# Performance work log

Hardware: AMD Instinct MI355X
Metric: run time of the kernel (lower is better)

## Reference

```python
import jax, jax.numpy as jnp
import numpy as np

HIDDEN = 1024
HEADS = 16
HEAD_DIM = HIDDEN // HEADS
SCALE = HEAD_DIM ** -0.5


def setup_inputs() -> dict:
    key = jax.random.key(0)
    kx, kw, ko = jax.random.split(key, 3)
    x = jax.random.normal(kx, (2, 2048, HIDDEN), dtype=jnp.float32)
    # nn.Linear(hidden, 3*hidden, bias=False): weight shape [3*hidden, hidden]
    w_qkv = jax.random.normal(kw, (3 * HIDDEN, HIDDEN), dtype=jnp.float32) * (HIDDEN ** -0.5)
    w_out = jax.random.normal(ko, (HIDDEN, HIDDEN), dtype=jnp.float32) * (HIDDEN ** -0.5)
    return {"x": x, "w_qkv": w_qkv, "w_out": w_out}


def reference(x, w_qkv, w_out):
    b, s, d = x.shape
    qkv = jnp.einsum('bsd,ed->bse', x, w_qkv)  # [b,s,3d]
    q, k, v = jnp.split(qkv, 3, axis=-1)
    def heads(t):
        return t.reshape(b, s, HEADS, HEAD_DIM).transpose(0, 2, 1, 3)  # [b,h,s,hd]
    q, k, v = heads(q), heads(k), heads(v)
    scores = jnp.einsum('bhqd,bhkd->bhqk', q, k) * SCALE
    attn = jax.nn.softmax(scores, axis=-1)
    out = jnp.einsum('bhqk,bhkd->bhqd', attn, v)
    out = out.transpose(0, 2, 1, 3).reshape(b, s, d)
    return jnp.einsum('bsd,ed->bse', out, w_out)
```

## Files before the change

### kernel.cpp

```cpp
#include <hip/hip_runtime.h>
#include <hip/hip_bf16.h>
#include <stdint.h>

typedef __bf16 bf16;
typedef __bf16 bf16x8 __attribute__((ext_vector_type(8)));
typedef float f32x4 __attribute__((ext_vector_type(4)));

#define HIDDEN 1024
#define HEADS  16
#define HD     64
#define SEQ    2048
#define BATCH  2
#define NTOK   (BATCH*SEQ)
#define E3     (3*HIDDEN)

#define QSCALE (0.125f * 1.44269504088896f)

#if __has_builtin(__builtin_amdgcn_exp2f)
#define EXP2(x) __builtin_amdgcn_exp2f(x)
#else
#define EXP2(x) __expf((x) * 0.69314718055995f)
#endif

static __device__ __forceinline__ uint32_t pkbf(float a, float b) {
  union { bf16 h[2]; uint32_t u; } x;
  x.h[0] = (bf16)a; x.h[1] = (bf16)b;
  return x.u;
}

__global__ __launch_bounds__(256) void k_convert(
    const float* __restrict__ x, const float* __restrict__ wqkv, const float* __restrict__ wout,
    bf16* __restrict__ xb, bf16* __restrict__ wqkvb, bf16* __restrict__ woutb)
{
  const int NX = NTOK*HIDDEN/4, NW = E3*HIDDEN/4;
  int i = blockIdx.x*256 + threadIdx.x;
  const float4* s; bf16* d; int o;
  if (i < NX)            { s=(const float4*)x;    d=xb;    o=i; }
  else if (i < NX+NW)    { s=(const float4*)wqkv; d=wqkvb; o=i-NX; }
  else                   { s=(const float4*)wout; d=woutb; o=i-NX-NW; }
  float4 v = s[o];
  union { bf16 b[4]; uint2 u; } p;
  p.b[0]=(bf16)v.x; p.b[1]=(bf16)v.y; p.b[2]=(bf16)v.z; p.b[3]=(bf16)v.w;
  *(uint2*)(d + (size_t)o*4) = p.u;
}

template<int EPI, int BM>
__global__ __launch_bounds__(256) void k_gemm(
    const bf16* __restrict__ A, const bf16* __restrict__ B,
    bf16* __restrict__ Oq, bf16* __restrict__ Ok, bf16* __restrict__ Ov,
    float* __restrict__ Of, int M, int N, int K, int nbn)
{
  constexpr int MI = BM/32;
  __shared__ bf16 As[BM*32];
  __shared__ bf16 Bs[128*32];
  const int t = threadIdx.x;
  const int lane = t & 63;
  const int w = t >> 6;
  const int g = lane >> 4;
  const int l15 = lane & 15;
  const int wm = (w >> 1) * (BM/2), wn = (w & 1) * 64;
  const int bm = blockIdx.x / nbn, bn = blockIdx.x % nbn;
  const int brow = bm*BM, bcol = bn*128;

  f32x4 acc[MI][4];
  #pragma unroll
  for (int mi=0;mi<MI;mi++)
    #pragma unroll
    for (int ni=0;ni<4;ni++)
      #pragma unroll
      for (int r=0;r<4;r++) acc[mi][ni][r] = 0.f;

  const int nk = K >> 5;
  for (int kt = 0; kt < nk; ++kt) {
    if constexpr (BM == 128) {
      int ch = w*128 + lane;
      const bf16* ga = A + (size_t)(brow + (ch>>2))*K + kt*32 + (ch&3)*8;
      __builtin_amdgcn_global_load_lds((const uint32_t*)ga, (uint32_t*)(As + (w*128)*8), 16, 0, 0);
      int ch2 = ch + 64;
      const bf16* ga2 = A + (size_t)(brow + (ch2>>2))*K + kt*32 + (ch2&3)*8;
      __builtin_amdgcn_global_load_lds((const uint32_t*)ga2, (uint32_t*)(As + (w*128+64)*8), 16, 0, 0);
    } else {
      int ch = w*64 + lane;
      const bf16* ga = A + (size_t)(brow + (ch>>2))*K + kt*32 + (ch&3)*8;
      __builtin_amdgcn_global_load_lds((const uint32_t*)ga, (uint32_t*)(As + (w*64)*8), 16, 0, 0);
    }
    {
      int ch = w*128 + lane;
      const bf16* gb = B + (size_t)(bcol + (ch>>2))*K + kt*32 + (ch&3)*8;
      __builtin_amdgcn_global_load_lds((const uint32_t*)gb, (uint32_t*)(Bs + (w*128)*8), 16, 0, 0);
      int ch2 = ch + 64;
      const bf16* gb2 = B + (size_t)(bcol + (ch2>>2))*K + kt*32 + (ch2&3)*8;
      __builtin_amdgcn_global_load_lds((const uint32_t*)gb2, (uint32_t*)(Bs + (w*128+64)*8), 16, 0, 0);
    }
    __syncthreads();
    bf16x8 af[MI], bfr[4];
    #pragma unroll
    for (int mi=0;mi<MI;mi++) af[mi]  = *(const bf16x8*)(As + (wm + mi*16 + l15)*32 + g*8);
    #pragma unroll
    for (int ni=0;ni<4;ni++) bfr[ni] = *(const bf16x8*)(Bs + (wn + ni*16 + l15)*32 + g*8);
    #pragma unroll
    for (int mi=0;mi<MI;mi++)
      #pragma unroll
      for (int ni=0;ni<4;ni++)
        acc[mi][ni] = __builtin_amdgcn_mfma_f32_16x16x32_bf16(af[mi], bfr[ni], acc[mi][ni], 0, 0, 0);
    __syncthreads();
  }

  #pragma unroll
  for (int mi=0;mi<MI;mi++) {
    #pragma unroll
    for (int ni=0;ni<4;ni++) {
      #pragma unroll
      for (int r=0;r<4;r++) {
        float val = acc[mi][ni][r];
        int m = brow + wm + mi*16 + 4*g + r;
        int e = bcol + wn + ni*16 + l15;
        if (EPI == 0) {
          int part = e >> 10, we = e & 1023;
          int hh = we >> 6, dd = we & 63;
          int b = m >> 11, sb = m & 2047;
          size_t idx = (((size_t)b*HEADS + hh)*SEQ + sb)*HD + dd;
          if (part == 0)      Oq[idx] = (bf16)(val * QSCALE);
          else if (part == 1) Ok[idx] = (bf16)val;
          else                Ov[idx] = (bf16)val;
        } else {
          Of[(size_t)m*HIDDEN + e] = val;
        }
      }
    }
  }
}

__global__ __launch_bounds__(256, 4) void k_attn(
    const bf16* __restrict__ Qg, const bf16* __restrict__ Kg, const bf16* __restrict__ Vg,
    bf16* __restrict__ Og)
{
  __shared__ bf16 Kl[64*64];
  __shared__ bf16 Vt[64*64];
  const int t = threadIdx.x;
  const int lane = t & 63;
  const int w = t >> 6;
  const int g = lane >> 4;
  const int q = lane & 15;
  const int bh = blockIdx.x >> 5;
  const int qb = blockIdx.x & 31;
  const int q0 = qb*64 + w*16;
  const size_t bhS = (size_t)bh * SEQ * HD;

  bf16x8 qf[2];
  {
    const bf16* qrow = Qg + bhS + (size_t)(q0 + q)*HD + 8*g;
    qf[0] = *(const bf16x8*)(qrow);
    qf[1] = *(const bf16x8*)(qrow + 32);
  }

  f32x4 ot[4];
  #pragma unroll
  for (int df=0;df<4;df++)
    #pragma unroll
    for (int r=0;r<4;r++) ot[df][r] = 0.f;
  float mrun = -3.0e38f, lrun = 0.f;

  const int kv0 = (t & 31)*2;
  const int dd0 = (t >> 5)*8;
  const int kvf0 = kv0 >> 4, gv = (kv0 >> 2) & 3, rv = kv0 & 3;
  const int pos0 = 32*(kvf0 >> 1) + 8*gv + 4*(kvf0 & 1) + rv;

  for (int it = 0; it < SEQ/64; ++it) {
    __syncthreads();
    {
      int ch = w*128 + lane;
      int row = ch>>3, o16 = ch&7;
      const bf16* gp = Kg + bhS + (size_t)(it*64+row)*HD + ((o16*8) ^ ((row&7)*8));
      __builtin_amdgcn_global_load_lds((const uint32_t*)gp, (uint32_t*)(Kl + (w*128)*8), 16, 0, 0);
      int ch2 = ch + 64;
      int row2 = ch2>>3, o16b = ch2&7;
      const bf16* gp2 = Kg + bhS + (size_t)(it*64+row2)*HD + ((o16b*8) ^ ((row2&7)*8));
      __builtin_amdgcn_global_load_lds((const uint32_t*)gp2, (uint32_t*)(Kl + (w*128+64)*8), 16, 0, 0);
    }
    {
      const bf16* vg = Vg + bhS + (size_t)(it*64 + kv0)*HD + dd0;
      uint4 va = *(const uint4*)vg;
      uint4 vb = *(const uint4*)(vg + HD);
      const uint32_t* pa = (const uint32_t*)&va;
      const uint32_t* pb = (const uint32_t*)&vb;
      #pragma unroll
      for (int jj=0;jj<8;jj++) {
        int dd = dd0 + jj;
        uint32_t pr = __builtin_amdgcn_perm(pb[jj>>1], pa[jj>>1],
                                            (jj&1) ? 0x07060302u : 0x05040100u);
        int byte = (dd*128 + pos0*2) ^ (jj<<4);
        *(uint32_t*)((char*)Vt + byte) = pr;
      }
    }
    __syncthreads();

    f32x4 sf[4];
    #pragma unroll
    for (int kvf=0;kvf<4;kvf++)
      #pragma unroll
      for (int r=0;r<4;r++) sf[kvf][r] = 0.f;
    #pragma unroll
    for (int kvf=0;kvf<4;kvf++) {
      int row = 16*kvf + q;
      #pragma unroll
      for (int kc=0;kc<2;kc++) {
        int byte = row*128 + (((16*g + 64*kc)) ^ ((row&7)<<4));
        bf16x8 kf = *(const bf16x8*)((const char*)Kl + byte);
        sf[kvf] = __builtin_amdgcn_mfma_f32_16x16x32_bf16(kf, qf[kc], sf[kvf], 0,0,0);
      }
    }

    float pm = -3.0e38f;
    #pragma unroll
    for (int kvf=0;kvf<4;kvf++)
      #pragma unroll
      for (int r=0;r<4;r++) pm = fmaxf(pm, sf[kvf][r]);
    pm = fmaxf(pm, __shfl_xor(pm, 16, 64));
    pm = fmaxf(pm, __shfl_xor(pm, 32, 64));

    if (__any(pm - mrun > 8.f)) {
      float mnew = fmaxf(mrun, pm);
      float alpha = EXP2(mrun - mnew);
      lrun *= alpha;
      #pragma unroll
      for (int df=0;df<4;df++)
        #pragma unroll
        for (int r=0;r<4;r++) ot[df][r] *= alpha;
      mrun = mnew;
    }
    float rs = 0.f;
    #pragma unroll
    for (int kvf=0;kvf<4;kvf++)
      #pragma unroll
      for (int r=0;r<4;r++) { float p = EXP2(sf[kvf][r]-mrun); sf[kvf][r]=p; rs += p; }
    rs += __shfl_xor(rs, 16, 64);
    rs += __shfl_xor(rs, 32, 64);
    lrun += rs;

    uint32_t pk[4][2];
    #pragma unroll
    for (int kvf=0;kvf<4;kvf++) {
      pk[kvf][0] = pkbf(sf[kvf][0], sf[kvf][1]);
      pk[kvf][1] = pkbf(sf[kvf][2], sf[kvf][3]);
    }

    #pragma unroll
    for (int kc=0;kc<2;kc++) {
      union { uint32_t u[4]; bf16x8 v; } pf;
      pf.u[0] = pk[2*kc][0]; pf.u[1] = pk[2*kc][1];
      pf.u[2] = pk[2*kc+1][0]; pf.u[3] = pk[2*kc+1][1];
      #pragma unroll
      for (int df=0;df<4;df++) {
        int row = 16*df + q;
        int byte = row*128 + (((16*g + 64*kc)) ^ ((row&7)<<4));
        bf16x8 vf = *(const bf16x8*)((const char*)Vt + byte);
        ot[df] = __builtin_amdgcn_mfma_f32_16x16x32_bf16(vf, pf.v, ot[df], 0,0,0);
      }
    }
  }

  float inv = 1.0f / lrun;
  int b = bh >> 4, head = bh & 15;
  size_t orow = ((size_t)b*SEQ + q0 + q)*HIDDEN + head*HD;
  #pragma unroll
  for (int df=0;df<4;df++) {
    uint2 pr;
    pr.x = pkbf(ot[df][0]*inv, ot[df][1]*inv);
    pr.y = pkbf(ot[df][2]*inv, ot[df][3]*inv);
    *(uint2*)(Og + orow + 16*df + 4*g) = pr;
  }
}

extern "C" void kernel_launch(void* const* d_in, const int* in_sizes, int n_in,
                              void* d_out, int out_size, void* d_ws, size_t ws_size,
                              hipStream_t stream)
{
  (void)in_sizes; (void)n_in; (void)out_size; (void)ws_size;
  const float* x    = (const float*)d_in[0];
  const float* wqkv = (const float*)d_in[1];
  const float* wout = (const float*)d_in[2];
  float* out = (float*)d_out;
  char* ws = (char*)d_ws;
  bf16* xb    = (bf16*)(ws);
  bf16* wqkvb = (bf16*)(ws + 8388608);
  bf16* woutb = (bf16*)(ws + 14680064);
  bf16* Q     = (bf16*)(ws + 16777216);
  bf16* K     = (bf16*)(ws + 25165824);
  bf16* V     = (bf16*)(ws + 33554432);
  bf16* O     = (bf16*)(ws + 41943040);

  k_convert<<<8192, 256, 0, stream>>>(x, wqkv, wout, xb, wqkvb, woutb);
  k_gemm<0,128><<<32*24, 256, 0, stream>>>(xb, wqkvb, Q, K, V, nullptr, NTOK, E3, HIDDEN, 24);
  k_attn<<<1024, 256, 0, stream>>>(Q, K, V, O);
  k_gemm<1,64><<<64*8, 256, 0, stream>>>(O, woutb, nullptr, nullptr, nullptr, out, NTOK, HIDDEN, HIDDEN, 8);
}
```

Before: 204.3 us.

## Double query rows per wave in attention and prefetch next K/V tile into registers

Each wave now handles 32 query rows instead of 16, so every K and V fragment read from LDS feeds two MFMAs and the block count is halved. The K load changes from direct global-to-LDS copies to register loads that are issued for the next tile right after the barrier, overlapping global latency with compute. In exchange the kernel uses more registers, with launch bounds lowered to 2 blocks per SM, and has fewer blocks in flight.

```diff
diff --git a/kernel.cpp b/kernel.cpp
--- a/kernel.cpp
+++ b/kernel.cpp
@@ -131,7 +131,7 @@
   }
 }
 
-__global__ __launch_bounds__(256, 4) void k_attn(
+__global__ __launch_bounds__(256, 2) void k_attn(
     const bf16* __restrict__ Qg, const bf16* __restrict__ Kg, const bf16* __restrict__ Vg,
     bf16* __restrict__ Og)
 {
@@ -142,133 +142,172 @@
   const int w = t >> 6;
   const int g = lane >> 4;
   const int q = lane & 15;
-  const int bh = blockIdx.x >> 5;
-  const int qb = blockIdx.x & 31;
-  const int q0 = qb*64 + w*16;
+  const int bh = blockIdx.x >> 4;
+  const int qb = blockIdx.x & 15;
+  const int q0 = qb*128 + w*32;
   const size_t bhS = (size_t)bh * SEQ * HD;
 
-  bf16x8 qf[2];
-  {
-    const bf16* qrow = Qg + bhS + (size_t)(q0 + q)*HD + 8*g;
-    qf[0] = *(const bf16x8*)(qrow);
-    qf[1] = *(const bf16x8*)(qrow + 32);
-  }
-
-  f32x4 ot[4];
-  #pragma unroll
-  for (int df=0;df<4;df++)
-    #pragma unroll
-    for (int r=0;r<4;r++) ot[df][r] = 0.f;
-  float mrun = -3.0e38f, lrun = 0.f;
-
+  bf16x8 qf[2][2];
+  #pragma unroll
+  for (int qs=0;qs<2;qs++) {
+    const bf16* qrow = Qg + bhS + (size_t)(q0 + 16*qs + q)*HD + 8*g;
+    qf[qs][0] = *(const bf16x8*)(qrow);
+    qf[qs][1] = *(const bf16x8*)(qrow + 32);
+  }
+
+  f32x4 ot[2][4];
+  #pragma unroll
+  for (int qs=0;qs<2;qs++)
+    #pragma unroll
+    for (int df=0;df<4;df++)
+      #pragma unroll
+      for (int r=0;r<4;r++) ot[qs][df][r] = 0.f;
+  float mrun0 = -3.0e38f, mrun1 = -3.0e38f, lrun0 = 0.f, lrun1 = 0.f;
+
+  const int kr0 = t >> 3, kp0 = t & 7;
   const int kv0 = (t & 31)*2;
   const int dd0 = (t >> 5)*8;
   const int kvf0 = kv0 >> 4, gv = (kv0 >> 2) & 3, rv = kv0 & 3;
   const int pos0 = 32*(kvf0 >> 1) + 8*gv + 4*(kvf0 & 1) + rv;
 
-  for (int it = 0; it < SEQ/64; ++it) {
+  auto loadK = [&](int it, uint4& a, uint4& b) {
+    const bf16* p0 = Kg + bhS + (size_t)(it*64 + kr0)*HD + kp0*8;
+    a = *(const uint4*)p0;
+    b = *(const uint4*)(p0 + 32*HD);
+  };
+  auto writeK = [&](uint4 a, uint4 b) {
+    int sw = (kp0 ^ (kr0 & 7)) * 16;
+    *(uint4*)((char*)Kl + kr0*128 + sw) = a;
+    *(uint4*)((char*)Kl + (kr0+32)*128 + sw) = b;
+  };
+  auto loadV = [&](int it, uint4& a, uint4& b) {
+    const bf16* vg = Vg + bhS + (size_t)(it*64 + kv0)*HD + dd0;
+    a = *(const uint4*)vg;
+    b = *(const uint4*)(vg + HD);
+  };
+  auto writeVt = [&](uint4 va, uint4 vb) {
+    const uint32_t* pa = (const uint32_t*)&va;
+    const uint32_t* pb = (const uint32_t*)&vb;
+    #pragma unroll
+    for (int jj=0;jj<8;jj++) {
+      int dd = dd0 + jj;
+      uint32_t pr = __builtin_amdgcn_perm(pb[jj>>1], pa[jj>>1],
+                                          (jj&1) ? 0x07060302u : 0x05040100u);
+      int byte = (dd*128 + pos0*2) ^ (jj<<4);
+      *(uint32_t*)((char*)Vt + byte) = pr;
+    }
+  };
+
+  uint4 ka, kb, va, vb;
+  loadK(0, ka, kb);
+  loadV(0, va, vb);
+
+  const int NT = SEQ/64;
+  for (int it = 0; it < NT; ++it) {
     __syncthreads();
-    {
-      int ch = w*128 + lane;
-      int row = ch>>3, o16 = ch&7;
-      const bf16* gp = Kg + bhS + (size_t)(it*64+row)*HD + ((o16*8) ^ ((row&7)*8));
-      __builtin_amdgcn_global_load_lds((const uint32_t*)gp, (uint32_t*)(Kl + (w*128)*8), 16, 0, 0);
-      int ch2 = ch + 64;
-      int row2 = ch2>>3, o16b = ch2&7;
-      const bf16* gp2 = Kg + bhS + (size_t)(it*64+row2)*HD + ((o16b*8) ^ ((row2&7)*8));
-      __builtin_amdgcn_global_load_lds((const uint32_t*)gp2, (uint32_t*)(Kl + (w*128+64)*8), 16, 0, 0);
-    }
-    {
-      const bf16* vg = Vg + bhS + (size_t)(it*64 + kv0)*HD + dd0;
-      uint4 va = *(const uint4*)vg;
-      uint4 vb = *(const uint4*)(vg + HD);
-      const uint32_t* pa = (const uint32_t*)&va;
-      const uint32_t* pb = (const uint32_t*)&vb;
-      #pragma unroll
-      for (int jj=0;jj<8;jj++) {
-        int dd = dd0 + jj;
-        uint32_t pr = __builtin_amdgcn_perm(pb[jj>>1], pa[jj>>1],
-                                            (jj&1) ? 0x07060302u : 0x05040100u);
-        int byte = (dd*128 + pos0*2) ^ (jj<<4);
-        *(uint32_t*)((char*)Vt + byte) = pr;
-      }
-    }
+    writeK(ka, kb);
+    writeVt(va, vb);
     __syncthreads();
-
-    f32x4 sf[4];
-    #pragma unroll
-    for (int kvf=0;kvf<4;kvf++)
-      #pragma unroll
-      for (int r=0;r<4;r++) sf[kvf][r] = 0.f;
+    if (it+1 < NT) {
+      loadK(it+1, ka, kb);
+      loadV(it+1, va, vb);
+    }
+
+    f32x4 sf[2][4];
+    #pragma unroll
+    for (int qs=0;qs<2;qs++)
+      #pragma unroll
+      for (int kvf=0;kvf<4;kvf++)
+        #pragma unroll
+        for (int r=0;r<4;r++) sf[qs][kvf][r] = 0.f;
     #pragma unroll
     for (int kvf=0;kvf<4;kvf++) {
       int row = 16*kvf + q;
       #pragma unroll
       for (int kc=0;kc<2;kc++) {
-        int byte = row*128 + (((16*g + 64*kc)) ^ ((row&7)<<4));
+        int byte = row*128 + ((16*g + 64*kc) ^ ((row&7)<<4));
         bf16x8 kf = *(const bf16x8*)((const char*)Kl + byte);
-        sf[kvf] = __builtin_amdgcn_mfma_f32_16x16x32_bf16(kf, qf[kc], sf[kvf], 0,0,0);
-      }
-    }
-
-    float pm = -3.0e38f;
+        sf[0][kvf] = __builtin_amdgcn_mfma_f32_16x16x32_bf16(kf, qf[0][kc], sf[0][kvf], 0,0,0);
+        sf[1][kvf] = __builtin_amdgcn_mfma_f32_16x16x32_bf16(kf, qf[1][kc], sf[1][kvf], 0,0,0);
+      }
+    }
+
+    float pm0 = -3.0e38f, pm1 = -3.0e38f;
     #pragma unroll
     for (int kvf=0;kvf<4;kvf++)
       #pragma unroll
-      for (int r=0;r<4;r++) pm = fmaxf(pm, sf[kvf][r]);
-    pm = fmaxf(pm, __shfl_xor(pm, 16, 64));
-    pm = fmaxf(pm, __shfl_xor(pm, 32, 64));
-
-    if (__any(pm - mrun > 8.f)) {
-      float mnew = fmaxf(mrun, pm);
-      float alpha = EXP2(mrun - mnew);
-      lrun *= alpha;
+      for (int r=0;r<4;r++) {
+        pm0 = fmaxf(pm0, sf[0][kvf][r]);
+        pm1 = fmaxf(pm1, sf[1][kvf][r]);
+      }
+    pm0 = fmaxf(pm0, __shfl_xor(pm0, 16, 64));
+    pm0 = fmaxf(pm0, __shfl_xor(pm0, 32, 64));
+    pm1 = fmaxf(pm1, __shfl_xor(pm1, 16, 64));
+    pm1 = fmaxf(pm1, __shfl_xor(pm1, 32, 64));
+
+    bool need = (pm0 - mrun0 > 8.f) || (pm1 - mrun1 > 8.f);
+    if (__any(need)) {
+      float mn0 = fmaxf(mrun0, pm0), mn1 = fmaxf(mrun1, pm1);
+      float a0 = EXP2(mrun0 - mn0), a1 = EXP2(mrun1 - mn1);
+      lrun0 *= a0; lrun1 *= a1;
       #pragma unroll
       for (int df=0;df<4;df++)
         #pragma unroll
-        for (int r=0;r<4;r++) ot[df][r] *= alpha;
-      mrun = mnew;
-    }
-    float rs = 0.f;
+        for (int r=0;r<4;r++) { ot[0][df][r] *= a0; ot[1][df][r] *= a1; }
+      mrun0 = mn0; mrun1 = mn1;
+    }
+    float rs0 = 0.f, rs1 = 0.f;
     #pragma unroll
     for (int kvf=0;kvf<4;kvf++)
       #pragma unroll
-      for (int r=0;r<4;r++) { float p = EXP2(sf[kvf][r]-mrun); sf[kvf][r]=p; rs += p; }
-    rs += __shfl_xor(rs, 16, 64);
-    rs += __shfl_xor(rs, 32, 64);
-    lrun += rs;
-
-    uint32_t pk[4][2];
-    #pragma unroll
-    for (int kvf=0;kvf<4;kvf++) {
-      pk[kvf][0] = pkbf(sf[kvf][0], sf[kvf][1]);
-      pk[kvf][1] = pkbf(sf[kvf][2], sf[kvf][3]);
-    }
+      for (int r=0;r<4;r++) {
+        float p0 = EXP2(sf[0][kvf][r] - mrun0); sf[0][kvf][r] = p0; rs0 += p0;
+        float p1 = EXP2(sf[1][kvf][r] - mrun1); sf[1][kvf][r] = p1; rs1 += p1;
+      }
+    rs0 += __shfl_xor(rs0, 16, 64); rs0 += __shfl_xor(rs0, 32, 64);
+    rs1 += __shfl_xor(rs1, 16, 64); rs1 += __shfl_xor(rs1, 32, 64);
+    lrun0 += rs0; lrun1 += rs1;
+
+    uint32_t pk[2][4][2];
+    #pragma unroll
+    for (int qs=0;qs<2;qs++)
+      #pragma unroll
+      for (int kvf=0;kvf<4;kvf++) {
+        pk[qs][kvf][0] = pkbf(sf[qs][kvf][0], sf[qs][kvf][1]);
+        pk[qs][kvf][1] = pkbf(sf[qs][kvf][2], sf[qs][kvf][3]);
+      }
 
     #pragma unroll
     for (int kc=0;kc<2;kc++) {
-      union { uint32_t u[4]; bf16x8 v; } pf;
-      pf.u[0] = pk[2*kc][0]; pf.u[1] = pk[2*kc][1];
-      pf.u[2] = pk[2*kc+1][0]; pf.u[3] = pk[2*kc+1][1];
+      union { uint32_t u[4]; bf16x8 v; } pf0, pf1;
+      pf0.u[0] = pk[0][2*kc][0]; pf0.u[1] = pk[0][2*kc][1];
+      pf0.u[2] = pk[0][2*kc+1][0]; pf0.u[3] = pk[0][2*kc+1][1];
+      pf1.u[0] = pk[1][2*kc][0]; pf1.u[1] = pk[1][2*kc][1];
+      pf1.u[2] = pk[1][2*kc+1][0]; pf1.u[3] = pk[1][2*kc+1][1];
       #pragma unroll
       for (int df=0;df<4;df++) {
         int row = 16*df + q;
-        int byte = row*128 + (((16*g + 64*kc)) ^ ((row&7)<<4));
+        int byte = row*128 + ((16*g + 64*kc) ^ ((row&7)<<4));
         bf16x8 vf = *(const bf16x8*)((const char*)Vt + byte);
-        ot[df] = __builtin_amdgcn_mfma_f32_16x16x32_bf16(vf, pf.v, ot[df], 0,0,0);
-      }
-    }
-  }
-
-  float inv = 1.0f / lrun;
+        ot[0][df] = __builtin_amdgcn_mfma_f32_16x16x32_bf16(vf, pf0.v, ot[0][df], 0,0,0);
+        ot[1][df] = __builtin_amdgcn_mfma_f32_16x16x32_bf16(vf, pf1.v, ot[1][df], 0,0,0);
+      }
+    }
+  }
+
+  float inv0 = 1.0f / lrun0, inv1 = 1.0f / lrun1;
   int b = bh >> 4, head = bh & 15;
-  size_t orow = ((size_t)b*SEQ + q0 + q)*HIDDEN + head*HD;
-  #pragma unroll
-  for (int df=0;df<4;df++) {
-    uint2 pr;
-    pr.x = pkbf(ot[df][0]*inv, ot[df][1]*inv);
-    pr.y = pkbf(ot[df][2]*inv, ot[df][3]*inv);
-    *(uint2*)(Og + orow + 16*df + 4*g) = pr;
+  #pragma unroll
+  for (int qs=0;qs<2;qs++) {
+    float inv = qs ? inv1 : inv0;
+    size_t orow = ((size_t)b*SEQ + q0 + 16*qs + q)*HIDDEN + head*HD;
+    #pragma unroll
+    for (int df=0;df<4;df++) {
+      uint2 pr;
+      pr.x = pkbf(ot[qs][df][0]*inv, ot[qs][df][1]*inv);
+      pr.y = pkbf(ot[qs][df][2]*inv, ot[qs][df][3]*inv);
+      *(uint2*)(Og + orow + 16*df + 4*g) = pr;
+    }
   }
 }
 
@@ -292,6 +331,6 @@
 
   k_convert<<<8192, 256, 0, stream>>>(x, wqkv, wout, xb, wqkvb, woutb);
   k_gemm<0,128><<<32*24, 256, 0, stream>>>(xb, wqkvb, Q, K, V, nullptr, NTOK, E3, HIDDEN, 24);
-  k_attn<<<1024, 256, 0, stream>>>(Q, K, V, O);
+  k_attn<<<512, 256, 0, stream>>>(Q, K, V, O);
   k_gemm<1,64><<<64*8, 256, 0, stream>>>(O, woutb, nullptr, nullptr, nullptr, out, NTOK, HIDDEN, HIDDEN, 8);
 }
```

Result: faster. 194.9 us (-4.6%).
